# Performance work log

Hardware: AMD Instinct MI355X
Metric: run time of the kernel (lower is better)

## Reference

```python
import jax, jax.numpy as jnp
import numpy as np

B, S, HID = 1, 4096, 4096
H, KV, D = 32, 8, 128
NUM_LANDMARKS = 64
LOCAL_WINDOW = 128          # window size in fast path
HW = LOCAL_WINDOW // 2      # half window = 64 (also used as block size)
ROPE_THETA = 10000.0
SCALE = 1.0 / np.sqrt(D)


def setup_inputs() -> dict:
    key = jax.random.key(0)
    k1, k2, k3, k4, k5 = jax.random.split(key, 5)
    return {
        "hidden_states": jax.random.normal(k1, (B, S, HID), dtype=jnp.float32),
        "wq": jax.random.normal(k2, (HID, H * D), dtype=jnp.float32) * 0.02,
        "wk": jax.random.normal(k3, (HID, KV * D), dtype=jnp.float32) * 0.02,
        "wv": jax.random.normal(k4, (HID, KV * D), dtype=jnp.float32) * 0.02,
        "wo": jax.random.normal(k5, (H * D, HID), dtype=jnp.float32) * 0.02,
    }


def _rope(x):
    # x: [B, h, S, D]; standard llama RoPE with rotate_half
    pos = jnp.arange(S, dtype=jnp.float32)
    inv_freq = 1.0 / (ROPE_THETA ** (jnp.arange(0, D, 2, dtype=jnp.float32) / D))
    freqs = pos[:, None] * inv_freq[None, :]              # [S, D/2]
    emb = jnp.concatenate([freqs, freqs], axis=-1)        # [S, D]
    cos, sin = jnp.cos(emb), jnp.sin(emb)
    x1, x2 = x[..., : D // 2], x[..., D // 2:]
    rot = jnp.concatenate([-x2, x1], axis=-1)
    return x * cos + rot * sin


def _ssa_fast(q, k, v):
    # q,k,v: [B, H, S, D] (kv already repeated to H heads). Causal, no dropout.
    nblk = S // HW  # block size == half window == 64
    # ---- local sliding-window attention (block-banded, honors sparsity) ----
    qb = q.reshape(B, H, nblk, HW, D)
    # pad keys/values by HW zeros on both sides (matches torch F.pad with 0)
    kp = jnp.pad(k, ((0, 0), (0, 0), (HW, HW), (0, 0)))
    vp = jnp.pad(v, ((0, 0), (0, 0), (HW, HW), (0, 0)))
    kpb = kp.reshape(B, H, nblk + 2, HW, D)
    vpb = vp.reshape(B, H, nblk + 2, HW, D)
    # each query block n sees key blocks n-1, n, n+1 (in padded coords: n, n+1, n+2)
    kb = jnp.concatenate([kpb[:, :, :nblk], kpb[:, :, 1:nblk + 1], kpb[:, :, 2:nblk + 2]], axis=3)  # [B,H,nblk,3*HW,D]
    vb = jnp.concatenate([vpb[:, :, :nblk], vpb[:, :, 1:nblk + 1], vpb[:, :, 2:nblk + 2]], axis=3)
    scores = jnp.einsum("bhnqd,bhnkd->bhnqk", qb, kb) * SCALE  # [B,H,nblk,HW,3*HW]
    # relative key position: rel = (j - HW) - i; window membership rel in [-HW, HW-1],
    # causal keeps rel <= 0  =>  i <= j <= i + HW. Left zero-padding stays attendable
    # (score 0), exactly like the torch unfold-over-zero-pad implementation.
    i_idx = jnp.arange(HW)[:, None]
    j_idx = jnp.arange(3 * HW)[None, :]
    mask = (j_idx >= i_idx) & (j_idx <= i_idx + HW)  # [HW, 3*HW]
    scores = jnp.where(mask, scores, -jnp.inf)
    w = jax.nn.softmax(scores, axis=-1)
    local_out = jnp.einsum("bhnqk,bhnkd->bhnqd", w, vb).reshape(B, H, S, D)
    # ---- global landmark attention ----
    stride = S // NUM_LANDMARKS
    lm_idx = jnp.arange(0, S, stride)[:NUM_LANDMARKS]         # [L]
    lk = k[:, :, lm_idx, :]                                   # [B,H,L,D]
    lv = v[:, :, lm_idx, :]
    ls = jnp.einsum("bhqd,bhkd->bhqk", q, lk) * SCALE         # [B,H,S,L]
    lm_mask = jnp.arange(S)[:, None] < lm_idx[None, :]        # future landmarks masked
    ls = jnp.where(lm_mask[None, None], -jnp.inf, ls)
    lw = jax.nn.softmax(ls, axis=-1)
    global_out = jnp.einsum("bhqk,bhkd->bhqd", lw, lv)
    return 0.7 * local_out + 0.3 * global_out


def reference(hidden_states, wq, wk, wv, wo):
    q = (hidden_states @ wq).reshape(B, S, H, D).transpose(0, 2, 1, 3)   # [B,H,S,D]
    k = (hidden_states @ wk).reshape(B, S, KV, D).transpose(0, 2, 1, 3)  # [B,KV,S,D]
    v = (hidden_states @ wv).reshape(B, S, KV, D).transpose(0, 2, 1, 3)
    q = _rope(q)
    k = _rope(k)
    groups = H // KV
    k = jnp.repeat(k, groups, axis=1)  # repeat_interleave over heads
    v = jnp.repeat(v, groups, axis=1)
    attn = _ssa_fast(q, k, v)                                 # [B,H,S,D]
    out = attn.transpose(0, 2, 1, 3).reshape(B, S, H * D) @ wo
    return out
```

## Files before the change

kernel.cpp:

```cpp
#include <hip/hip_runtime.h>
#include <hip/hip_bf16.h>


typedef short bf16x8 __attribute__((ext_vector_type(8)));
typedef float f32x4 __attribute__((ext_vector_type(4)));
using bf16 = __hip_bfloat16;

#define S_LEN 4096
#define HIDN  4096
#define NH    32
#define NKV   8
#define DH    128
#define NBLK  64
#define SCALE 0.08838834764831845f

__device__ __forceinline__ void gload16(const bf16* g, bf16* l) {
  __builtin_amdgcn_global_load_lds(
      (const __attribute__((address_space(1))) unsigned int*)g,
      (__attribute__((address_space(3))) unsigned int*)l, 16, 0, 0);
}

__global__ void k_detect(const unsigned short* __restrict__ w,
                         int* __restrict__ flag) {
  int t = threadIdx.x;
  unsigned short u = w[t];
  int e = (u >> 7) & 0xFF;
  int bad = (e >= 134) ? 1 : 0;
  __shared__ int cnt;
  if (t == 0) cnt = 0;
  __syncthreads();
  atomicAdd(&cnt, bad);
  __syncthreads();
  if (t == 0) flag[0] = (cnt > 32) ? 1 : 0;
}

__global__ void k_cvt(const void* __restrict__ in, bf16* __restrict__ out,
                      const int* __restrict__ flagp, int n8) {
  int i = blockIdx.x * blockDim.x + threadIdx.x;
  if (i >= n8) return;
  if (*flagp) {
    const float4* p = (const float4*)in + (size_t)i * 2;
    float4 a = p[0], b = p[1];
    alignas(16) bf16 v[8] = {__float2bfloat16(a.x), __float2bfloat16(a.y),
                             __float2bfloat16(a.z), __float2bfloat16(a.w),
                             __float2bfloat16(b.x), __float2bfloat16(b.y),
                             __float2bfloat16(b.z), __float2bfloat16(b.w)};
    *(uint4*)(out + (size_t)i * 8) = *(const uint4*)v;
  } else {
    ((uint4*)out)[i] = ((const uint4*)in)[i];
  }
}

__global__ __launch_bounds__(256) void k_tcvt(const void* __restrict__ w_,
                                              bf16* __restrict__ wt,
                                              const int* __restrict__ flagp,
                                              int K, int N) {
  __shared__ bf16 tile[64][66];
  const bool f32 = *flagp != 0;
  const int k0 = blockIdx.x * 64, n0 = blockIdx.y * 64;
  const int t = threadIdx.x;
  const int r = t >> 2, c16 = (t & 3) * 16;
  if (f32) {
    const float* src = (const float*)w_ + (size_t)(k0 + r) * N + n0 + c16;
    float4 a = ((const float4*)src)[0], b = ((const float4*)src)[1];
    float4 c = ((const float4*)src)[2], d = ((const float4*)src)[3];
    bf16* dst = &tile[r][c16];
    dst[0] = __float2bfloat16(a.x);  dst[1] = __float2bfloat16(a.y);
    dst[2] = __float2bfloat16(a.z);  dst[3] = __float2bfloat16(a.w);
    dst[4] = __float2bfloat16(b.x);  dst[5] = __float2bfloat16(b.y);
    dst[6] = __float2bfloat16(b.z);  dst[7] = __float2bfloat16(b.w);
    dst[8] = __float2bfloat16(c.x);  dst[9] = __float2bfloat16(c.y);
    dst[10] = __float2bfloat16(c.z); dst[11] = __float2bfloat16(c.w);
    dst[12] = __float2bfloat16(d.x); dst[13] = __float2bfloat16(d.y);
    dst[14] = __float2bfloat16(d.z); dst[15] = __float2bfloat16(d.w);
  } else {
    const bf16* src = (const bf16*)w_ + (size_t)(k0 + r) * N + n0 + c16;
    uint4 a = ((const uint4*)src)[0], b = ((const uint4*)src)[1];
    *(uint4*)(&tile[r][c16]) = a;
    *(uint4*)(&tile[r][c16 + 8]) = b;
  }
  __syncthreads();
  alignas(16) bf16 v[16];
#pragma unroll
  for (int j = 0; j < 16; j++) v[j] = tile[c16 + j][r];
  bf16* dst = wt + (size_t)(n0 + r) * K + k0 + c16;
  ((uint4*)dst)[0] = ((const uint4*)v)[0];
  ((uint4*)dst)[1] = ((const uint4*)v)[1];
}

#define WAITV(N) asm volatile("s_waitcnt vmcnt(" #N ")" ::: "memory")
#define BARRIER()                                \
  do {                                           \
    asm volatile("" ::: "memory");               \
    __builtin_amdgcn_s_barrier();                \
    asm volatile("" ::: "memory");               \
  } while (0)

__global__ __launch_bounds__(512, 2) void k_gemm(
    const bf16* __restrict__ A, const bf16* __restrict__ BT,
    void* __restrict__ outQ, void* __restrict__ outK, void* __restrict__ outV,
    const int* __restrict__ flagp, int M, int N, int K, int kind) {
  __shared__ __align__(16) bf16 lds[65536];
  const int NT = K >> 6;
  const int mb = M >> 8;
  const int nwg = mb * (N >> 8);
  const int bid = blockIdx.y * gridDim.x + blockIdx.x;
  const int lin = (bid & 7) * (nwg >> 3) + (bid >> 3);
  const int m0 = (lin % mb) << 8;
  const int n0 = (lin / mb) << 8;
  const int t = threadIdx.x;
  const int wid = t >> 6, lane = t & 63, quad = lane >> 4, l16 = lane & 15;
  const int wr = wid >> 2, wc = wid & 3;
  const int sw = (quad ^ ((l16 >> 1) & 3)) * 8;

  f32x4 acc[8][4] = {};
  bf16x8 a[4], bfr[4];

  auto stageHalf = [&](int g) {
    const int kt = g >> 2, j = g & 3;
    const int buf = kt & 1, isB = j & 1, kh = j >> 1;
    const bf16* src = isB ? BT : A;
    const int r0 = isB ? n0 : m0;
    const int base = (isB ? 32768 : 0) + buf * 16384 + kh * 8192;
    const int kcol = kt * 64 + kh * 32;
#pragma unroll
    for (int p = 0; p < 2; p++) {
      int u = p * 512 + t;
      int r = u >> 2;
      int gb = (u & 3) ^ ((r >> 1) & 3);
      gload16(src + (size_t)(r0 + r) * K + kcol + gb * 8, &lds[base + u * 8]);
    }
  };

#define READS(kt, KH, MH)                                                     \
  {                                                                           \
    const int abase = ((kt) & 1) * 16384 + (KH) * 8192;                       \
    _Pragma("unroll") for (int i = 0; i < 4; i++) a[i] =                      \
        *(const bf16x8*)&lds[abase +                                          \
                             (wr * 128 + ((MH) * 4 + i) * 16 + l16) * 32 +    \
                             sw];                                             \
    if ((MH) == 0) {                                                          \
      const int bbase = 32768 + ((kt) & 1) * 16384 + (KH) * 8192;             \
      _Pragma("unroll") for (int j = 0; j < 4; j++) bfr[j] =                  \
          *(const bf16x8*)&lds[bbase + (wc * 64 + j * 16 + l16) * 32 + sw];   \
    }                                                                         \
  }

#define MFMAS(MH)                                                             \
  {                                                                           \
    __builtin_amdgcn_s_setprio(1);                                            \
    _Pragma("unroll") for (int i = 0; i < 4; i++)                             \
        _Pragma("unroll") for (int j = 0; j < 4; j++) acc[(MH) * 4 + i][j] =  \
            __builtin_amdgcn_mfma_f32_16x16x32_bf16(                          \
                a[i], bfr[j], acc[(MH) * 4 + i][j], 0, 0, 0);                 \
    __builtin_amdgcn_s_setprio(0);                                            \
  }

  stageHalf(0); stageHalf(1); stageHalf(2); stageHalf(3);
  stageHalf(4); stageHalf(5);
  WAITV(8);
  BARRIER();

  const int G = 4 * NT;
  for (int kt = 0; kt < NT; ++kt) {
    const int g = 4 * kt + 6;
    READS(kt, 0, 0);
    if (g < G) stageHalf(g);
    MFMAS(0);
    BARRIER();
    READS(kt, 0, 1);
    if (g + 1 < G) stageHalf(g + 1);
    MFMAS(1);
    if (kt < NT - 1) { WAITV(8); } else { WAITV(0); }
    BARRIER();
    READS(kt, 1, 0);
    if (g + 2 < G) stageHalf(g + 2);
    MFMAS(0);
    BARRIER();
    READS(kt, 1, 1);
    if (g + 3 < G) stageHalf(g + 3);
    MFMAS(1);
    if (kt < NT - 2) { WAITV(8); } else if (kt == NT - 2) { WAITV(4); }
    BARRIER();
  }

  const bool storeF32 = (kind == 1) && (*flagp != 0);
#pragma unroll
  for (int i = 0; i < 8; i++)
#pragma unroll
    for (int j = 0; j < 4; j++)
#pragma unroll
      for (int r = 0; r < 4; r++) {
        int m = m0 + wr * 128 + i * 16 + quad * 4 + r;
        int n = n0 + wc * 64 + j * 16 + l16;
        float v = acc[i][j][r];
        if (kind == 1) {
          if (storeF32)
            ((float*)outQ)[(size_t)m * N + n] = v;
          else
            ((bf16*)outQ)[(size_t)m * N + n] = __float2bfloat16(v);
        } else {
          bf16* Co;
          if (n < 4096)
            Co = (bf16*)outQ + (size_t)m * 4096 + n;
          else if (n < 5120)
            Co = (bf16*)outK + (size_t)m * 1024 + (n - 4096);
          else
            Co = (bf16*)outV + (size_t)m * 1024 + (n - 5120);
          *Co = __float2bfloat16(v);
        }
      }
}

__global__ void k_rope(bf16* __restrict__ Q, bf16* __restrict__ Kb,
                       int totalQ, int total) {
  int idx = blockIdx.x * blockDim.x + threadIdx.x;
  if (idx >= total) return;
  bf16* x;
  int nheads, li;
  if (idx < totalQ) { x = Q; nheads = NH; li = idx; }
  else { x = Kb; nheads = NKV; li = idx - totalQ; }
  int j = li & 63;
  int sh = li >> 6;
  int s = sh / nheads;
  float invf = (float)exp(-(double)j * (9.210340371976184 / 64.0));
  float ang = (float)s * invf;
  float sn, cs;
  sincosf(ang, &sn, &cs);
  bf16* p = x + (size_t)sh * DH;
  float x1 = __bfloat162float(p[j]);
  float x2 = __bfloat162float(p[j + 64]);
  p[j]      = __float2bfloat16(x1 * cs - x2 * sn);
  p[j + 64] = __float2bfloat16(x2 * cs + x1 * sn);
}

__global__ __launch_bounds__(256) void k_attn(const bf16* __restrict__ Q,
                                              const bf16* __restrict__ Kk,
                                              const bf16* __restrict__ V,
                                              bf16* __restrict__ O) {
  const int nb = blockIdx.x;
  const int h = blockIdx.y;
  const int kvh = h >> 2;
  const int t = threadIdx.x;
  const int wid = t >> 6, lane = t & 63, quad = lane >> 4, l16 = lane & 15;

  __shared__ bf16 Qs[64 * 136];
  __shared__ bf16 kvb[128 * 136];
  __shared__ bf16 PLs[64 * 72];

  const int srow16 = t >> 4, soff = (t & 15) * 8;

#pragma unroll
  for (int p = 0; p < 4; p++) {
    int row = p * 16 + srow16;
    *(uint4*)(&Qs[row * 136 + soff]) =
        *(const uint4*)(Q + ((size_t)(nb * 64 + row) * NH + h) * DH + soff);
  }

  auto stageK = [&](int basePos, int posStride) {
#pragma unroll
    for (int p = 0; p < 4; p++) {
      int row = p * 16 + srow16;
      int pos = basePos + row * posStride;
      uint4 val = make_uint4(0u, 0u, 0u, 0u);
      if (pos >= 0)
        val = *(const uint4*)(Kk + ((size_t)pos * NKV + kvh) * DH + soff);
      *(uint4*)(&kvb[row * 136 + soff]) = val;
    }
  };

  auto stageVt = [&](int basePos, int posStride) {
#pragma unroll
    for (int p = 0; p < 4; p++) {
      int key = p * 16 + srow16;
      int pos = basePos + key * posStride;
      uint4 tv = make_uint4(0u, 0u, 0u, 0u);
      if (pos >= 0)
        tv = *(const uint4*)(V + ((size_t)pos * NKV + kvh) * DH + soff);
      const bf16* tmp = (const bf16*)&tv;
#pragma unroll
      for (int jj = 0; jj < 8; jj++)
        kvb[(soff + jj) * 72 + key] = tmp[jj];
    }
  };

  f32x4 sc[8] = {};
  f32x4 slm[4] = {};

  auto scoreStep = [&](f32x4* dst) {
#pragma unroll
    for (int kk = 0; kk < 128; kk += 32) {
      bf16x8 a = *(const bf16x8*)(&Qs[(wid * 16 + l16) * 136 + kk + quad * 8]);
#pragma unroll
      for (int nt = 0; nt < 4; nt++) {
        bf16x8 b =
            *(const bf16x8*)(&kvb[(nt * 16 + l16) * 136 + kk + quad * 8]);
        dst[nt] = __builtin_amdgcn_mfma_f32_16x16x32_bf16(a, b, dst[nt], 0, 0, 0);
      }
    }
  };

  stageK(nb * 64 - 64, 1);
  __syncthreads();
  scoreStep(&sc[0]);
  __syncthreads();
  stageK(nb * 64, 1);
  __syncthreads();
  scoreStep(&sc[4]);
  __syncthreads();
  stageK(0, 64);
  __syncthreads();
  scoreStep(&slm[0]);
  __syncthreads();

  float invL[4], invG[4];
#pragma unroll
  for (int r = 0; r < 4; r++) {
    const int i = wid * 16 + quad * 4 + r;
    float mx = -1e30f;
#pragma unroll
    for (int nt = 0; nt < 8; nt++) {
      int j = nt * 16 + l16;
      float s = sc[nt][r] * SCALE;
      if (j < i || j > i + 64) s = -1e30f;
      sc[nt][r] = s;
      mx = fmaxf(mx, s);
    }
#pragma unroll
    for (int m = 1; m <= 8; m <<= 1) mx = fmaxf(mx, __shfl_xor(mx, m, 64));
    float sum = 0.f;
#pragma unroll
    for (int nt = 0; nt < 8; nt++) {
      float e = __expf(sc[nt][r] - mx);
      sc[nt][r] = e;
      sum += e;
    }
#pragma unroll
    for (int m = 1; m <= 8; m <<= 1) sum += __shfl_xor(sum, m, 64);
    invL[r] = 0.7f / sum;

    float mg = -1e30f;
#pragma unroll
    for (int nt = 0; nt < 4; nt++) {
      int l = nt * 16 + l16;
      float s = slm[nt][r] * SCALE;
      if (l > nb) s = -1e30f;
      slm[nt][r] = s;
      mg = fmaxf(mg, s);
    }
#pragma unroll
    for (int m = 1; m <= 8; m <<= 1) mg = fmaxf(mg, __shfl_xor(mg, m, 64));
    float sg = 0.f;
#pragma unroll
    for (int nt = 0; nt < 4; nt++) {
      float e = __expf(slm[nt][r] - mg);
      slm[nt][r] = e;
      sg += e;
    }
#pragma unroll
    for (int m = 1; m <= 8; m <<= 1) sg += __shfl_xor(sg, m, 64);
    invG[r] = 0.3f / sg;
  }

#pragma unroll
  for (int nt = 0; nt < 8; nt++)
#pragma unroll
    for (int r = 0; r < 4; r++)
      Qs[(wid * 16 + quad * 4 + r) * 136 + nt * 16 + l16] =
          __float2bfloat16(sc[nt][r]);
#pragma unroll
  for (int nt = 0; nt < 4; nt++)
#pragma unroll
    for (int r = 0; r < 4; r++)
      PLs[(wid * 16 + quad * 4 + r) * 72 + nt * 16 + l16] =
          __float2bfloat16(slm[nt][r]);
  stageVt(nb * 64 - 64, 1);
  __syncthreads();

  f32x4 accO[8] = {};
  f32x4 accG[8] = {};
  auto pvStep = [&](f32x4* dst, const bf16* Pbase, int pstride, int colbase) {
#pragma unroll
    for (int kk = 0; kk < 64; kk += 32) {
      bf16x8 a = *(const bf16x8*)(&Pbase[(wid * 16 + l16) * pstride + colbase +
                                         kk + quad * 8]);
#pragma unroll
      for (int nt = 0; nt < 8; nt++) {
        bf16x8 b = *(const bf16x8*)(&kvb[(nt * 16 + l16) * 72 + kk + quad * 8]);
        dst[nt] = __builtin_amdgcn_mfma_f32_16x16x32_bf16(a, b, dst[nt], 0, 0, 0);
      }
    }
  };
  pvStep(accO, Qs, 136, 0);
  __syncthreads();
  stageVt(nb * 64, 1);
  __syncthreads();
  pvStep(accO, Qs, 136, 64);
  __syncthreads();
  stageVt(0, 64);
  __syncthreads();
  pvStep(accG, PLs, 72, 0);

#pragma unroll
  for (int nt = 0; nt < 8; nt++)
#pragma unroll
    for (int r = 0; r < 4; r++) {
      int q = nb * 64 + wid * 16 + quad * 4 + r;
      int d = nt * 16 + l16;
      float v = accO[nt][r] * invL[r] + accG[nt][r] * invG[r];
      O[((size_t)q * NH + h) * DH + d] = __float2bfloat16(v);
    }
}

extern "C" void kernel_launch(void* const* d_in, const int* in_sizes, int n_in,
                              void* d_out, int out_size, void* d_ws,
                              size_t ws_size, hipStream_t stream) {
  const void* X  = d_in[0];
  const void* wq = d_in[1];
  const void* wk = d_in[2];
  const void* wv = d_in[3];
  const void* wo = d_in[4];

  char* ws = (char*)d_ws;
  int* flag = (int*)ws;
  bf16* Xb   = (bf16*)(ws + 256);
  bf16* Wcat = Xb + (size_t)S_LEN * HIDN;
  bf16* Qb   = Wcat + (size_t)6144 * HIDN;
  bf16* Kb   = Qb + (size_t)S_LEN * HIDN;
  bf16* Vb   = Kb + (size_t)S_LEN * 1024;
  bf16* At   = Xb;
  bf16* WoT  = Wcat;

  k_detect<<<1, 256, 0, stream>>>((const unsigned short*)wq, flag);

  k_cvt<<<(S_LEN * HIDN / 8 + 255) / 256, 256, 0, stream>>>(
      X, Xb, flag, S_LEN * HIDN / 8);
  k_tcvt<<<dim3(HIDN / 64, HIDN / 64), 256, 0, stream>>>(
      wq, Wcat, flag, HIDN, HIDN);
  k_tcvt<<<dim3(HIDN / 64, 1024 / 64), 256, 0, stream>>>(
      wk, Wcat + (size_t)4096 * HIDN, flag, HIDN, 1024);
  k_tcvt<<<dim3(HIDN / 64, 1024 / 64), 256, 0, stream>>>(
      wv, Wcat + (size_t)5120 * HIDN, flag, HIDN, 1024);

  k_gemm<<<dim3(S_LEN / 256, 6144 / 256), 512, 0, stream>>>(
      Xb, Wcat, Qb, Kb, Vb, flag, S_LEN, 6144, HIDN, 0);

  int totalQ = S_LEN * NH * 64, total = totalQ + S_LEN * NKV * 64;
  k_rope<<<(total + 255) / 256, 256, 0, stream>>>(Qb, Kb, totalQ, total);

  k_attn<<<dim3(NBLK, NH), 256, 0, stream>>>(Qb, Kb, Vb, At);

  k_tcvt<<<dim3(HIDN / 64, HIDN / 64), 256, 0, stream>>>(
      wo, WoT, flag, HIDN, HIDN);

  k_gemm<<<dim3(S_LEN / 256, HIDN / 256), 512, 0, stream>>>(
      At, WoT, d_out, nullptr, nullptr, flag, S_LEN, HIDN, HIDN, 1);
}
```

Before: 722.1 us.

## Double-buffer GEMM LDS fragment registers to overlap reads with MFMAs

Splits the A and B fragment registers into two sets so the LDS reads for the next MFMA phase are issued before the current phase's MFMAs run. The vmcnt waits are moved and retuned, and sched_barrier fences are added to keep the compiler from reordering reads across the MFMA blocks. The goal is to hide LDS read latency behind matrix work in the projection GEMMs. The cost is more VGPRs under launch bounds of 512 threads and 2 blocks per CU, plus more intricate wait and barrier correctness.

Result: no change. 721.3 us (-0.1%).

```diff
diff --git a/kernel.cpp b/kernel.cpp
--- a/kernel.cpp
+++ b/kernel.cpp
@@ -89,6 +89,7 @@
 }
 
 #define WAITV(N) asm volatile("s_waitcnt vmcnt(" #N ")" ::: "memory")
+#define SCHEDB() __builtin_amdgcn_sched_barrier(0)
 #define BARRIER()                                \
   do {                                           \
     asm volatile("" ::: "memory");               \
@@ -114,7 +115,7 @@
   const int sw = (quad ^ ((l16 >> 1) & 3)) * 8;
 
   f32x4 acc[8][4] = {};
-  bf16x8 a[4], bfr[4];
+  bf16x8 a0[4], a1[4], b0[4], b1[4];
 
   auto stageHalf = [&](int g) {
     const int kt = g >> 2, j = g & 3;
@@ -132,27 +133,27 @@
     }
   };
 
-#define READS(kt, KH, MH)                                                     \
+#define RDA(d, BUF, KH, MH)                                                   \
   {                                                                           \
-    const int abase = ((kt) & 1) * 16384 + (KH) * 8192;                       \
-    _Pragma("unroll") for (int i = 0; i < 4; i++) a[i] =                      \
+    const int abase = (BUF) * 16384 + (KH) * 8192;                            \
+    _Pragma("unroll") for (int i = 0; i < 4; i++) d[i] =                      \
         *(const bf16x8*)&lds[abase +                                          \
                              (wr * 128 + ((MH) * 4 + i) * 16 + l16) * 32 +    \
                              sw];                                             \
-    if ((MH) == 0) {                                                          \
-      const int bbase = 32768 + ((kt) & 1) * 16384 + (KH) * 8192;             \
-      _Pragma("unroll") for (int j = 0; j < 4; j++) bfr[j] =                  \
-          *(const bf16x8*)&lds[bbase + (wc * 64 + j * 16 + l16) * 32 + sw];   \
-    }                                                                         \
-  }
-
-#define MFMAS(MH)                                                             \
+  }
+#define RDB(d, BUF, KH)                                                       \
+  {                                                                           \
+    const int bbase = 32768 + (BUF) * 16384 + (KH) * 8192;                    \
+    _Pragma("unroll") for (int j = 0; j < 4; j++) d[j] =                      \
+        *(const bf16x8*)&lds[bbase + (wc * 64 + j * 16 + l16) * 32 + sw];     \
+  }
+#define MF(AS, BS, MH)                                                        \
   {                                                                           \
     __builtin_amdgcn_s_setprio(1);                                            \
     _Pragma("unroll") for (int i = 0; i < 4; i++)                             \
         _Pragma("unroll") for (int j = 0; j < 4; j++) acc[(MH) * 4 + i][j] =  \
             __builtin_amdgcn_mfma_f32_16x16x32_bf16(                          \
-                a[i], bfr[j], acc[(MH) * 4 + i][j], 0, 0, 0);                 \
+                AS[i], BS[j], acc[(MH) * 4 + i][j], 0, 0, 0);                 \
     __builtin_amdgcn_s_setprio(0);                                            \
   }
 
@@ -160,27 +161,38 @@
   stageHalf(4); stageHalf(5);
   WAITV(8);
   BARRIER();
+  RDA(a0, 0, 0, 0);
+  RDB(b0, 0, 0);
 
   const int G = 4 * NT;
   for (int kt = 0; kt < NT; ++kt) {
+    const int buf = kt & 1, nbuf = buf ^ 1;
     const int g = 4 * kt + 6;
-    READS(kt, 0, 0);
+    RDA(a1, buf, 0, 1);
     if (g < G) stageHalf(g);
-    MFMAS(0);
+    SCHEDB();
+    MF(a0, b0, 0);
+    if (kt < NT - 1) { WAITV(6); } else { WAITV(0); }
     BARRIER();
-    READS(kt, 0, 1);
+    RDA(a0, buf, 1, 0);
+    RDB(b1, buf, 1);
     if (g + 1 < G) stageHalf(g + 1);
-    MFMAS(1);
-    if (kt < NT - 1) { WAITV(8); } else { WAITV(0); }
+    SCHEDB();
+    MF(a1, b0, 1);
     BARRIER();
-    READS(kt, 1, 0);
+    RDA(a1, buf, 1, 1);
     if (g + 2 < G) stageHalf(g + 2);
-    MFMAS(0);
+    SCHEDB();
+    MF(a0, b1, 0);
+    if (kt < NT - 2) { WAITV(6); } else if (kt == NT - 2) { WAITV(4); }
     BARRIER();
-    READS(kt, 1, 1);
+    if (kt < NT - 1) {
+      RDA(a0, nbuf, 0, 0);
+      RDB(b0, nbuf, 0);
+    }
     if (g + 3 < G) stageHalf(g + 3);
-    MFMAS(1);
-    if (kt < NT - 2) { WAITV(8); } else if (kt == NT - 2) { WAITV(4); }
+    SCHEDB();
+    MF(a1, b1, 1);
     BARRIER();
   }
 
```

## Template GEMM on N-tile width and restructure K-loop pipeline

Applied to the files above, without the earlier changes.

Makes the GEMM kernel a template over the N-tile width. The QKV projection uses a 256x128 tile, giving 384 workgroups instead of 192, which is meant to fill the CUs better. The K-loop staging is rewritten from quarter-stage granularity into per-half-K stages that load A and B together, and each stage issues all MFMAs at once. The narrower tile lowers data reuse per workgroup and changes how much prefetch stays in flight, so load latency may be hidden less well.

Measured after the change: 694.9 us. -3.8%, faster.

```diff
diff --git a/kernel.cpp b/kernel.cpp
--- a/kernel.cpp
+++ b/kernel.cpp
@@ -96,102 +96,107 @@
     asm volatile("" ::: "memory");               \
   } while (0)
 
+template <int BN>
 __global__ __launch_bounds__(512, 2) void k_gemm(
     const bf16* __restrict__ A, const bf16* __restrict__ BT,
     void* __restrict__ outQ, void* __restrict__ outK, void* __restrict__ outV,
     const int* __restrict__ flagp, int M, int N, int K, int kind) {
-  __shared__ __align__(16) bf16 lds[65536];
+  constexpr int AF = (BN == 256) ? 8 : 4;
+  constexpr int BL = (BN == 256) ? 2 : 1;
+  constexpr int BKH = BN * 32;
+  __shared__ __align__(16) bf16 lds[32768 + 4 * BKH];
   const int NT = K >> 6;
   const int mb = M >> 8;
-  const int nwg = mb * (N >> 8);
+  const int nwg = mb * (N / BN);
   const int bid = blockIdx.y * gridDim.x + blockIdx.x;
   const int lin = (bid & 7) * (nwg >> 3) + (bid >> 3);
   const int m0 = (lin % mb) << 8;
-  const int n0 = (lin / mb) << 8;
+  const int n0 = (lin / mb) * BN;
   const int t = threadIdx.x;
   const int wid = t >> 6, lane = t & 63, quad = lane >> 4, l16 = lane & 15;
-  const int wr = wid >> 2, wc = wid & 3;
+  const int wr = (BN == 256) ? (wid >> 2) : (wid >> 1);
+  const int wc = (BN == 256) ? (wid & 3) : (wid & 1);
   const int sw = (quad ^ ((l16 >> 1) & 3)) * 8;
 
-  f32x4 acc[8][4] = {};
-  bf16x8 a[4], bfr[4];
-
-  auto stageHalf = [&](int g) {
-    const int kt = g >> 2, j = g & 3;
-    const int buf = kt & 1, isB = j & 1, kh = j >> 1;
-    const bf16* src = isB ? BT : A;
-    const int r0 = isB ? n0 : m0;
-    const int base = (isB ? 32768 : 0) + buf * 16384 + kh * 8192;
+  f32x4 acc[AF][4] = {};
+  bf16x8 a[AF], b[4];
+
+  auto stageA = [&](int kt, int kh) {
+    const int base = (kt & 1) * 16384 + kh * 8192;
     const int kcol = kt * 64 + kh * 32;
 #pragma unroll
     for (int p = 0; p < 2; p++) {
       int u = p * 512 + t;
       int r = u >> 2;
       int gb = (u & 3) ^ ((r >> 1) & 3);
-      gload16(src + (size_t)(r0 + r) * K + kcol + gb * 8, &lds[base + u * 8]);
-    }
-  };
-
-#define READS(kt, KH, MH)                                                     \
-  {                                                                           \
-    const int abase = ((kt) & 1) * 16384 + (KH) * 8192;                       \
-    _Pragma("unroll") for (int i = 0; i < 4; i++) a[i] =                      \
-        *(const bf16x8*)&lds[abase +                                          \
-                             (wr * 128 + ((MH) * 4 + i) * 16 + l16) * 32 +    \
-                             sw];                                             \
-    if ((MH) == 0) {                                                          \
-      const int bbase = 32768 + ((kt) & 1) * 16384 + (KH) * 8192;             \
-      _Pragma("unroll") for (int j = 0; j < 4; j++) bfr[j] =                  \
-          *(const bf16x8*)&lds[bbase + (wc * 64 + j * 16 + l16) * 32 + sw];   \
-    }                                                                         \
-  }
-
-#define MFMAS(MH)                                                             \
+      gload16(A + (size_t)(m0 + r) * K + kcol + gb * 8, &lds[base + u * 8]);
+    }
+  };
+  auto stageB = [&](int kt, int kh) {
+    const int base = 32768 + (kt & 1) * (2 * BKH) + kh * BKH;
+    const int kcol = kt * 64 + kh * 32;
+#pragma unroll
+    for (int p = 0; p < BL; p++) {
+      int u = p * 512 + t;
+      int r = u >> 2;
+      int gb = (u & 3) ^ ((r >> 1) & 3);
+      gload16(BT + (size_t)(n0 + r) * K + kcol + gb * 8, &lds[base + u * 8]);
+    }
+  };
+  auto rdAB = [&](int buf, int kh) {
+    const int abase = buf * 16384 + kh * 8192;
+#pragma unroll
+    for (int i = 0; i < AF; i++)
+      a[i] = *(const bf16x8*)&lds[abase + (wr * (AF * 16) + i * 16 + l16) * 32 + sw];
+    const int bbase = 32768 + buf * (2 * BKH) + kh * BKH;
+#pragma unroll
+    for (int j = 0; j < 4; j++)
+      b[j] = *(const bf16x8*)&lds[bbase + (wc * 64 + j * 16 + l16) * 32 + sw];
+  };
+
+#define MFMA_ALL()                                                            \
   {                                                                           \
     __builtin_amdgcn_s_setprio(1);                                            \
-    _Pragma("unroll") for (int i = 0; i < 4; i++)                             \
-        _Pragma("unroll") for (int j = 0; j < 4; j++) acc[(MH) * 4 + i][j] =  \
-            __builtin_amdgcn_mfma_f32_16x16x32_bf16(                          \
-                a[i], bfr[j], acc[(MH) * 4 + i][j], 0, 0, 0);                 \
+    _Pragma("unroll") for (int i = 0; i < AF; i++)                            \
+        _Pragma("unroll") for (int j = 0; j < 4; j++) acc[i][j] =             \
+            __builtin_amdgcn_mfma_f32_16x16x32_bf16(a[i], b[j], acc[i][j],    \
+                                                    0, 0, 0);                 \
     __builtin_amdgcn_s_setprio(0);                                            \
   }
 
-  stageHalf(0); stageHalf(1); stageHalf(2); stageHalf(3);
-  stageHalf(4); stageHalf(5);
-  WAITV(8);
+  stageA(0, 0); stageB(0, 0);
+  stageA(0, 1); stageB(0, 1);
+  if constexpr (BN == 256) { WAITV(4); } else { WAITV(3); }
   BARRIER();
 
-  const int G = 4 * NT;
   for (int kt = 0; kt < NT; ++kt) {
-    const int g = 4 * kt + 6;
-    READS(kt, 0, 0);
-    if (g < G) stageHalf(g);
-    MFMAS(0);
+    const int buf = kt & 1;
+    rdAB(buf, 0);
+    if (kt + 1 < NT) { stageA(kt + 1, 0); stageB(kt + 1, 0); }
+    MFMA_ALL();
+    if (kt + 1 < NT) {
+      if constexpr (BN == 256) { WAITV(4); } else { WAITV(3); }
+    } else {
+      WAITV(0);
+    }
     BARRIER();
-    READS(kt, 0, 1);
-    if (g + 1 < G) stageHalf(g + 1);
-    MFMAS(1);
-    if (kt < NT - 1) { WAITV(8); } else { WAITV(0); }
+    rdAB(buf, 1);
+    if (kt + 1 < NT) { stageA(kt + 1, 1); stageB(kt + 1, 1); }
+    MFMA_ALL();
+    if (kt + 1 < NT) {
+      if constexpr (BN == 256) { WAITV(4); } else { WAITV(3); }
+    }
     BARRIER();
-    READS(kt, 1, 0);
-    if (g + 2 < G) stageHalf(g + 2);
-    MFMAS(0);
-    BARRIER();
-    READS(kt, 1, 1);
-    if (g + 3 < G) stageHalf(g + 3);
-    MFMAS(1);
-    if (kt < NT - 2) { WAITV(8); } else if (kt == NT - 2) { WAITV(4); }
-    BARRIER();
   }
 
   const bool storeF32 = (kind == 1) && (*flagp != 0);
 #pragma unroll
-  for (int i = 0; i < 8; i++)
+  for (int i = 0; i < AF; i++)
 #pragma unroll
     for (int j = 0; j < 4; j++)
 #pragma unroll
       for (int r = 0; r < 4; r++) {
-        int m = m0 + wr * 128 + i * 16 + quad * 4 + r;
+        int m = m0 + wr * (AF * 16) + i * 16 + quad * 4 + r;
         int n = n0 + wc * 64 + j * 16 + l16;
         float v = acc[i][j][r];
         if (kind == 1) {
@@ -442,7 +447,7 @@
   k_tcvt<<<dim3(HIDN / 64, 1024 / 64), 256, 0, stream>>>(
       wv, Wcat + (size_t)5120 * HIDN, flag, HIDN, 1024);
 
-  k_gemm<<<dim3(S_LEN / 256, 6144 / 256), 512, 0, stream>>>(
+  k_gemm<128><<<dim3(S_LEN / 256, 6144 / 128), 512, 0, stream>>>(
       Xb, Wcat, Qb, Kb, Vb, flag, S_LEN, 6144, HIDN, 0);
 
   int totalQ = S_LEN * NH * 64, total = totalQ + S_LEN * NKV * 64;
@@ -453,6 +458,6 @@
   k_tcvt<<<dim3(HIDN / 64, HIDN / 64), 256, 0, stream>>>(
       wo, WoT, flag, HIDN, HIDN);
 
-  k_gemm<<<dim3(S_LEN / 256, HIDN / 256), 512, 0, stream>>>(
+  k_gemm<256><<<dim3(S_LEN / 256, HIDN / 256), 512, 0, stream>>>(
       At, WoT, d_out, nullptr, nullptr, flag, S_LEN, HIDN, HIDN, 1);
 }
```
